# Kernel optimization log

Hardware: AMD Instinct MI355X
Metric: run time of the kernel (lower is better)

## Reference

```python
import jax, jax.numpy as jnp
import numpy as np

DIM = 1536
NHEADS = 12
HDIM = DIM // NHEADS  # 128
EPS = 1e-6
LOCAL_ATTN_SIZE = 3
SINK_SIZE = 1
MAX_ATTN = 32760 if LOCAL_ATTN_SIZE == -1 else LOCAL_ATTN_SIZE * 1560  # 4680


def _rms(x, g):
    # WanRMSNorm over last dim
    return x * jax.lax.rsqrt(jnp.mean(x * x, axis=-1, keepdims=True) + EPS) * g


def _rope(x, f, h, w, fr, fi, start_frame):
    # x: [b, s, n, d] with s == f*h*w; fr/fi: [1024, d//2] real/imag of complex rotations
    b, s, n, d = x.shape
    c = d // 2
    c0 = c - 2 * (c // 3)
    c1 = c // 3
    fc = jax.lax.complex(fr, fi)  # [1024, c]
    xr = x.reshape(b, s, n, c, 2)
    xc = jax.lax.complex(xr[..., 0], xr[..., 1])  # [b, s, n, c]
    ff = fc[start_frame:start_frame + f, :c0]      # [f, c0]
    fh = fc[:h, c0:c0 + c1]                        # [h, c1]
    fw = fc[:w, c0 + c1:c0 + 2 * c1]               # [w, c1]
    freqs_i = jnp.concatenate([
        jnp.broadcast_to(ff[:, None, None, :], (f, h, w, c0)),
        jnp.broadcast_to(fh[None, :, None, :], (f, h, w, c1)),
        jnp.broadcast_to(fw[None, None, :, :], (f, h, w, c1)),
    ], axis=-1).reshape(1, s, 1, c)
    y = xc * freqs_i
    return jnp.stack([y.real, y.imag], axis=-1).reshape(b, s, n, d)


def _attn(q, k, v):
    # plain SDPA (decode path of the module uses no mask on the gathered window)
    scale = 1.0 / np.sqrt(q.shape[-1]).astype(np.float32)
    logits = jnp.einsum('bqnd,bknd->bnqk', q, k) * scale
    p = jax.nn.softmax(logits, axis=-1)
    return jnp.einsum('bnqk,bknd->bqnd', p, v)


def _forward(x, cache_k, cache_v, freqs_real, freqs_imag,
             wq, bq, wk, bk, wv, bv, wo, bo, gq, gk,
             f_frames, height, width, current_start, global_end_index, local_end_index):
    b, s, _ = x.shape
    n, d = NHEADS, HDIM
    frame_seqlen = height * width
    start_frame = current_start // frame_seqlen

    q = _rms(x @ wq + bq, gq).reshape(b, s, n, d)
    k = _rms(x @ wk + bk, gk).reshape(b, s, n, d)
    v = (x @ wv + bv).reshape(b, s, n, d)

    rq = _rope(q, f_frames, height, width, freqs_real, freqs_imag, start_frame)
    rk = _rope(k, f_frames, height, width, freqs_real, freqs_imag, start_frame)

    current_end = current_start + s
    sink_tokens = SINK_SIZE * frame_seqlen
    kv_size = cache_k.shape[1]
    is_recompute = (current_end <= global_end_index) and (current_start > 0)

    kc, vc = cache_k, cache_v
    if LOCAL_ATTN_SIZE != -1 and current_end > global_end_index and s + local_end_index > kv_size:
        # evict oldest non-sink tokens, roll the rest toward the sink region
        num_evicted = s + local_end_index - kv_size
        num_rolled = local_end_index - num_evicted - sink_tokens
        src = slice(sink_tokens + num_evicted, sink_tokens + num_evicted + num_rolled)
        kc = kc.at[:, sink_tokens:sink_tokens + num_rolled].set(jax.lax.stop_gradient(cache_k[:, src]))
        vc = vc.at[:, sink_tokens:sink_tokens + num_rolled].set(jax.lax.stop_gradient(cache_v[:, src]))
        new_local_end = local_end_index + current_end - global_end_index - num_evicted
    else:
        new_local_end = local_end_index + current_end - global_end_index
    local_start = new_local_end - s
    write_start = max(local_start, sink_tokens) if is_recompute else local_start
    off = max(0, write_start - local_start)
    wl = max(0, new_local_end - write_start)
    if wl > 0:
        kc = kc.at[:, write_start:new_local_end].set(rk[:, off:off + wl])
        vc = vc.at[:, write_start:new_local_end].set(v[:, off:off + wl])

    if sink_tokens > 0:
        budget = MAX_ATTN - sink_tokens
        if budget > 0:
            lo = max(sink_tokens, new_local_end - budget)
            kcat = jnp.concatenate([kc[:, :sink_tokens], kc[:, lo:new_local_end]], axis=1)
            vcat = jnp.concatenate([vc[:, :sink_tokens], vc[:, lo:new_local_end]], axis=1)
        else:
            kcat, vcat = kc[:, :sink_tokens], vc[:, :sink_tokens]
        o = _attn(rq, kcat, vcat)
    else:
        ws = max(0, new_local_end - MAX_ATTN)
        o = _attn(rq, kc[:, ws:new_local_end], vc[:, ws:new_local_end])

    return o.reshape(b, s, DIM) @ wo + bo


def setup_inputs() -> dict:
    key = jax.random.key(0)
    ks = jax.random.split(key, 12)
    B, S, CACHE = 1, 1560, 4680
    sc = 0.02
    # RoPE tables as unit-magnitude complex rotations
    ang = jax.random.uniform(ks[0], (1024, HDIM // 2), jnp.float32, 0.0, 2.0 * np.pi)
    return {
        'x': jax.random.normal(ks[1], (B, S, DIM), jnp.float32),
        'cache_k': jax.random.normal(ks[2], (B, CACHE, NHEADS, HDIM), jnp.float32),
        'cache_v': jax.random.normal(ks[3], (B, CACHE, NHEADS, HDIM), jnp.float32),
        'freqs_real': jnp.cos(ang),
        'freqs_imag': jnp.sin(ang),
        'wq': jax.random.normal(ks[4], (DIM, DIM), jnp.float32) * sc,
        'bq': jnp.zeros((DIM,), jnp.float32),
        'wk': jax.random.normal(ks[5], (DIM, DIM), jnp.float32) * sc,
        'bk': jnp.zeros((DIM,), jnp.float32),
        'wv': jax.random.normal(ks[6], (DIM, DIM), jnp.float32) * sc,
        'bv': jnp.zeros((DIM,), jnp.float32),
        'wo': jax.random.normal(ks[7], (DIM, DIM), jnp.float32) * sc,
        'bo': jnp.zeros((DIM,), jnp.float32),
        'gq': jnp.ones((DIM,), jnp.float32),
        'gk': jnp.ones((DIM,), jnp.float32),
        'f_frames': 1,
        'height': 30,
        'width': 52,
        'current_start': 4680,
        'global_end_index': 4680,
        'local_end_index': 4680,
    }


def reference(x, cache_k, cache_v, freqs_real, freqs_imag,
              wq, bq, wk, bk, wv, bv, wo, bo, gq, gk,
              f_frames, height, width, current_start, global_end_index, local_end_index):
    return _forward(x, cache_k, cache_v, freqs_real, freqs_imag,
                    wq, bq, wk, bk, wv, bv, wo, bo, gq, gk,
                    f_frames, height, width, current_start, global_end_index, local_end_index)
```

## Files before the change

### kernel.cpp

```cpp
#include <hip/hip_runtime.h>
#include <cstdint>
#include <cstddef>

typedef unsigned int  u32;
typedef unsigned short u16;
typedef short s16x8 __attribute__((ext_vector_type(8)));
typedef float f32x4 __attribute__((ext_vector_type(4)));

#define DIM     1536
#define NH      12
#define HD      128
#define SEQ     1560
#define MPAD    1664
#define NKV     4680
#define NKPAD   4736
#define ROLL0   3120
#define NQK     4608
#define START_FRAME 3
#define NEGINF  -3.0e4f
#define NSPLIT  5
#define SPLITKC 960

#define EXP2F(x) exp2f(x)

__device__ __forceinline__ u16 f2bf(float f){
  u32 u = __builtin_bit_cast(u32, f);
  u32 r = (u + 0x7fffu + ((u >> 16) & 1u)) >> 16;
  return (u16)r;
}

__global__ void k_pre(const float* __restrict__ x, u16* __restrict__ xp,
                      u16* __restrict__ Kc, u16* __restrict__ VT,
                      u16* __restrict__ Qr, u16* __restrict__ Opad,
                      float* __restrict__ sumsq){
  int b = blockIdx.x;
  if (b < 244){
    int i = b * 256 + threadIdx.x;
    uint4 z = make_uint4(0u, 0u, 0u, 0u);
    if (i < 10752){
      int h = i / 896, r = i % 896;
      ((uint4*)(Kc + ((size_t)h * NKPAD + NKV) * 128))[r] = z;
    } else if (i < 21504){
      int j = i - 10752; int row = j / 7, c = j % 7;
      ((uint4*)(VT + (size_t)row * NKPAD + NKV))[c] = z;
    } else if (i < 41472){
      int j = i - 21504; int h = j / 1664, r = j % 1664;
      ((uint4*)(Qr + ((size_t)h * MPAD + SEQ) * 128))[r] = z;
    } else if (i < 61440){
      int r = i - 41472;
      ((uint4*)(Opad + (size_t)SEQ * DIM))[r] = z;
    } else if (i < 62272){
      ((uint4*)sumsq)[i - 61440] = z;
    }
  } else {
    int i = (b - 244) * 256 + threadIdx.x;
    const int n_src = SEQ * DIM / 8;
    u16 o[8] = {0,0,0,0,0,0,0,0};
    if (i < n_src){
      float4 a = ((const float4*)x)[2*i];
      float4 c = ((const float4*)x)[2*i + 1];
      o[0]=f2bf(a.x); o[1]=f2bf(a.y); o[2]=f2bf(a.z); o[3]=f2bf(a.w);
      o[4]=f2bf(c.x); o[5]=f2bf(c.y); o[6]=f2bf(c.z); o[7]=f2bf(c.w);
    }
    uint4 v = make_uint4((u32)o[0]|((u32)o[1]<<16), (u32)o[2]|((u32)o[3]<<16),
                         (u32)o[4]|((u32)o[5]<<16), (u32)o[6]|((u32)o[7]<<16));
    ((uint4*)xp)[i] = v;
  }
}

__global__ void k_transpose_w(const float* __restrict__ wq, const float* __restrict__ wk,
                              const float* __restrict__ wv, const float* __restrict__ wo,
                              u16* __restrict__ WTqkv, u16* __restrict__ WTo){
  __shared__ u32 tile[64][65];
  int z = blockIdx.z;
  const float* w = (z==0)?wq:(z==1)?wk:(z==2)?wv:wo;
  u16* dst = (z < 3) ? (WTqkv + (size_t)z * DIM * DIM) : WTo;
  int r0 = blockIdx.x * 64, c0 = blockIdx.y * 64;
  int t = threadIdx.x;
  int rr = t >> 4, cg = t & 15;
#pragma unroll
  for (int i = 0; i < 4; i++){
    int r = rr + i * 16;
    float4 v = *(const float4*)(w + (size_t)(r0 + r) * DIM + c0 + cg * 4);
    tile[r][cg*4+0] = f2bf(v.x); tile[r][cg*4+1] = f2bf(v.y);
    tile[r][cg*4+2] = f2bf(v.z); tile[r][cg*4+3] = f2bf(v.w);
  }
  __syncthreads();
  int c = t >> 2, rg = t & 3;
  u32 wds[8];
#pragma unroll
  for (int j = 0; j < 8; j++)
    wds[j] = (tile[rg*16 + 2*j][c] & 0xffffu) | (tile[rg*16 + 2*j + 1][c] << 16);
  u16* q = dst + (size_t)(c0 + c) * DIM + r0 + rg * 16;
  *(uint4*)q       = make_uint4(wds[0], wds[1], wds[2], wds[3]);
  *(uint4*)(q + 8) = make_uint4(wds[4], wds[5], wds[6], wds[7]);
}

#define LDK 40
__global__ __launch_bounds__(256) void k_gemm_qkv(
    const u16* __restrict__ A, const u16* __restrict__ B,
    const float* __restrict__ biasq, const float* __restrict__ biask, const float* __restrict__ biasv,
    float* __restrict__ Y, float* __restrict__ sumsq){
  __shared__ u16 As[128*LDK];
  __shared__ u16 Bs[128*LDK];
  int m0 = blockIdx.y * 128, n0 = blockIdx.x * 128;
  int t = threadIdx.x, w = t >> 6, lane = t & 63, quad = lane >> 4, lc = lane & 15;
  int wm = w & 1, wn = w >> 1;
  int sr = t >> 1, sh = (t & 1) * 16;
  f32x4 acc[4][4] = {};
  for (int kt = 0; kt < DIM/32; kt++){
    int k0 = kt * 32;
    __syncthreads();
    {
      const uint4* ga = (const uint4*)(A + (size_t)(m0 + sr) * DIM + k0 + sh);
      uint4 a0 = ga[0], a1 = ga[1];
      const uint4* gb = (const uint4*)(B + (size_t)(n0 + sr) * DIM + k0 + sh);
      uint4 b0 = gb[0], b1 = gb[1];
      *(uint4*)(As + sr * LDK + sh)     = a0;
      *(uint4*)(As + sr * LDK + sh + 8) = a1;
      *(uint4*)(Bs + sr * LDK + sh)     = b0;
      *(uint4*)(Bs + sr * LDK + sh + 8) = b1;
    }
    __syncthreads();
    s16x8 af[4], bf[4];
#pragma unroll
    for (int mt = 0; mt < 4; mt++) af[mt] = *(const s16x8*)(As + (wm*64 + mt*16 + lc) * LDK + quad * 8);
#pragma unroll
    for (int nt = 0; nt < 4; nt++) bf[nt] = *(const s16x8*)(Bs + (wn*64 + nt*16 + lc) * LDK + quad * 8);
#pragma unroll
    for (int mt = 0; mt < 4; mt++)
#pragma unroll
      for (int nt = 0; nt < 4; nt++)
        acc[mt][nt] = __builtin_amdgcn_mfma_f32_16x16x32_bf16(af[mt], bf[nt], acc[mt][nt], 0, 0, 0);
  }
  const float* bias; int cbase; int which;
  if (n0 < DIM)        { bias = biasq; cbase = 0;     which = 0; }
  else if (n0 < 2*DIM) { bias = biask; cbase = DIM;   which = 1; }
  else                 { bias = biasv; cbase = 2*DIM; which = 2; }
  float bvals[4];
#pragma unroll
  for (int nt = 0; nt < 4; nt++) bvals[nt] = bias[n0 - cbase + wn*64 + nt*16 + lc];
#pragma unroll
  for (int mt = 0; mt < 4; mt++){
    int row0 = m0 + wm*64 + mt*16 + quad*4;
    float ss[4] = {0.f, 0.f, 0.f, 0.f};
#pragma unroll
    for (int nt = 0; nt < 4; nt++){
      int col = n0 + wn*64 + nt*16 + lc;
#pragma unroll
      for (int r = 0; r < 4; r++){
        float y = acc[mt][nt][r] + bvals[nt];
        Y[(size_t)(row0 + r) * NQK + col] = y;
        ss[r] += y * y;
      }
    }
    if (which < 2){
      float* dst = sumsq + (which ? MPAD : 0);
#pragma unroll
      for (int r = 0; r < 4; r++){
        float v = ss[r];
        v += __shfl_xor(v, 1); v += __shfl_xor(v, 2); v += __shfl_xor(v, 4); v += __shfl_xor(v, 8);
        if (lc == 0) atomicAdd(&dst[row0 + r], v);
      }
    }
  }
}

__global__ void k_rope_qk(const float* __restrict__ Y, const float* __restrict__ sumsq,
                          const float* __restrict__ gq, const float* __restrict__ gk,
                          const float* __restrict__ fre, const float* __restrict__ fim,
                          u16* __restrict__ Qr, u16* __restrict__ Kc){
  int pos = blockIdx.x;
  int t = threadIdx.x;
  float scq = rsqrtf(sumsq[pos]        * (1.0f/1536.0f) + 1e-6f);
  float sck = rsqrtf(sumsq[MPAD + pos] * (1.0f/1536.0f) + 1e-6f);
  int hrow = pos / 52, wrow = pos % 52;
#pragma unroll
  for (int i = 0; i < 3; i++){
    int p = t + i * 256;
    int head = p >> 6, j = p & 63;
    int frow = (j < 22) ? START_FRAME : ((j < 43) ? hrow : wrow);
    float cr = fre[frow * 64 + j], ci = fim[frow * 64 + j];
    int d0 = head * 128 + 2 * j;
    float2 yq = *(const float2*)(Y + (size_t)pos * NQK + d0);
    float qa = yq.x * scq * gq[d0];
    float qb = yq.y * scq * gq[d0 + 1];
    u32 oq = (u32)f2bf(qa * cr - qb * ci) | ((u32)f2bf(qa * ci + qb * cr) << 16);
    *(u32*)(Qr + (size_t)(head * MPAD + pos) * 128 + 2 * j) = oq;
    float2 yk = *(const float2*)(Y + (size_t)pos * NQK + DIM + d0);
    float ka = yk.x * sck * gk[d0];
    float kb = yk.y * sck * gk[d0 + 1];
    u32 ok = (u32)f2bf(ka * cr - kb * ci) | ((u32)f2bf(ka * ci + kb * cr) << 16);
    *(u32*)(Kc + (size_t)(head * NKPAD + ROLL0 + pos) * 128 + 2 * j) = ok;
  }
}

__global__ void k_copy_cache_k(const float* __restrict__ ck, u16* __restrict__ Kc){
  int p = blockIdx.x;
  int src = (p < SEQ) ? p : p + SEQ;
  int t = threadIdx.x;
  int h = t >> 4, d = (t & 15) * 8;
  const float* s = ck + (size_t)src * DIM + t * 8;
  float4 a = ((const float4*)s)[0], b = ((const float4*)s)[1];
  uint4 v = make_uint4((u32)f2bf(a.x)|((u32)f2bf(a.y)<<16), (u32)f2bf(a.z)|((u32)f2bf(a.w)<<16),
                       (u32)f2bf(b.x)|((u32)f2bf(b.y)<<16), (u32)f2bf(b.z)|((u32)f2bf(b.w)<<16));
  *(uint4*)(Kc + (size_t)(h * NKPAD + p) * 128 + d) = v;
}

__global__ void k_tv_cache(const float* __restrict__ cv, u16* __restrict__ VT){
  __shared__ u32 tile[64][65];
  int p0 = blockIdx.x * 64, hd0 = blockIdx.y * 64;
  int t = threadIdx.x;
  int pr = t >> 4, cg = t & 15;
#pragma unroll
  for (int i = 0; i < 4; i++){
    int p = p0 + pr + i * 16;
    if (p < ROLL0){
      int src = (p < SEQ) ? p : p + SEQ;
      float4 v = *(const float4*)(cv + (size_t)src * DIM + hd0 + cg * 4);
      tile[pr + i*16][cg*4+0] = f2bf(v.x); tile[pr + i*16][cg*4+1] = f2bf(v.y);
      tile[pr + i*16][cg*4+2] = f2bf(v.z); tile[pr + i*16][cg*4+3] = f2bf(v.w);
    }
  }
  __syncthreads();
  int hd = t >> 2, pg = t & 3;
  int pbase = p0 + pg * 16;
  if (pbase < ROLL0){
    u32 wds[8];
#pragma unroll
    for (int j = 0; j < 8; j++)
      wds[j] = (tile[pg*16 + 2*j][hd] & 0xffffu) | (tile[pg*16 + 2*j + 1][hd] << 16);
    u16* q = VT + (size_t)(hd0 + hd) * NKPAD + pbase;
    *(uint4*)q       = make_uint4(wds[0], wds[1], wds[2], wds[3]);
    *(uint4*)(q + 8) = make_uint4(wds[4], wds[5], wds[6], wds[7]);
  }
}

__global__ void k_tv_new(const float* __restrict__ Y, u16* __restrict__ VT){
  __shared__ u32 tile[64][65];
  int p0 = blockIdx.x * 64, hd0 = blockIdx.y * 64;
  int t = threadIdx.x;
  int pr = t >> 4, cg = t & 15;
#pragma unroll
  for (int i = 0; i < 4; i++){
    int p = p0 + pr + i * 16;
    if (p < SEQ){
      float4 v = *(const float4*)(Y + (size_t)p * NQK + 2*DIM + hd0 + cg * 4);
      tile[pr + i*16][cg*4+0] = f2bf(v.x); tile[pr + i*16][cg*4+1] = f2bf(v.y);
      tile[pr + i*16][cg*4+2] = f2bf(v.z); tile[pr + i*16][cg*4+3] = f2bf(v.w);
    }
  }
  __syncthreads();
  int hd = t >> 2, pg = t & 3;
  int pbase = p0 + pg * 16;
  u32 wds[8];
#pragma unroll
  for (int j = 0; j < 8; j++)
    wds[j] = (tile[pg*16 + 2*j][hd] & 0xffffu) | (tile[pg*16 + 2*j + 1][hd] << 16);
  u16* q = VT + (size_t)(hd0 + hd) * NKPAD + ROLL0 + pbase;
  if (pbase + 8  <= SEQ) *(uint4*)q       = make_uint4(wds[0], wds[1], wds[2], wds[3]);
  if (pbase + 16 <= SEQ) *(uint4*)(q + 8) = make_uint4(wds[4], wds[5], wds[6], wds[7]);
}

#define LDKS 136
#define LDVS 68
#define LDPS 76
#define DEFER_THR 12.0f
__global__ __launch_bounds__(512, 4) void k_attn(const u16* __restrict__ Qr, const u16* __restrict__ Kc,
                                                 const u16* __restrict__ VT,
                                                 float* __restrict__ Opart, float* __restrict__ ml){
  __shared__ u16 Ks[64 * LDKS];
  __shared__ u16 Vs[128 * LDVS];
  __shared__ u16 Ps[8][16 * LDPS];
  int h = blockIdx.y, qb = blockIdx.x, sp = blockIdx.z;
  int t = threadIdx.x, w = t >> 6, lane = t & 63, quad = lane >> 4, lc = lane & 15;
  int qbase = qb * 128 + w * 16;
  const u16* Qbase = Qr + (size_t)(h * MPAD + qbase + lc) * 128;
  s16x8 qf[4];
#pragma unroll
  for (int kk = 0; kk < 4; kk++) qf[kk] = *(const s16x8*)(Qbase + kk * 32 + quad * 8);
  f32x4 oacc[8] = {};
  float m_[4] = {NEGINF, NEGINF, NEGINF, NEGINF};
  float l_[4] = {0.f, 0.f, 0.f, 0.f};
  const float scale = 0.08838834764831845f * 1.4426950408889634f;
  const u16* Kh = Kc + (size_t)h * NKPAD * 128;
  const u16* Vh = VT + (size_t)h * 128 * NKPAD;
  u16* Pw = &Ps[w][0];
  int kr0 = t >> 4,          kg0 = (t & 15) * 8;
  int kr1 = (t + 512) >> 4,  kg1 = ((t + 512) & 15) * 8;
  int vd0 = t >> 3,          vp0 = (t & 7) * 8;
  int vd1 = (t + 512) >> 3,  vp1 = ((t + 512) & 7) * 8;

  int kc0 = sp * SPLITKC;
  int kc1 = (sp == NSPLIT-1) ? NKPAD : kc0 + SPLITKC;
  uint4 kp0, kp1, vp0r, vp1r;
  {
    int kc = kc0;
    kp0  = *(const uint4*)(Kh + (size_t)(kc + kr0) * 128 + kg0);
    kp1  = *(const uint4*)(Kh + (size_t)(kc + kr1) * 128 + kg1);
    vp0r = *(const uint4*)(Vh + (size_t)vd0 * NKPAD + kc + vp0);
    vp1r = *(const uint4*)(Vh + (size_t)vd1 * NKPAD + kc + vp1);
  }
  for (int kc = kc0; kc < kc1; kc += 64){
    __syncthreads();
    *(uint4*)(Ks + kr0 * LDKS + kg0) = kp0;
    *(uint4*)(Ks + kr1 * LDKS + kg1) = kp1;
    *(uint4*)(Vs + vd0 * LDVS + vp0) = vp0r;
    *(uint4*)(Vs + vd1 * LDVS + vp1) = vp1r;
    __syncthreads();
    if (kc + 64 < kc1){
      int kn = kc + 64;
      kp0  = *(const uint4*)(Kh + (size_t)(kn + kr0) * 128 + kg0);
      kp1  = *(const uint4*)(Kh + (size_t)(kn + kr1) * 128 + kg1);
      vp0r = *(const uint4*)(Vh + (size_t)vd0 * NKPAD + kn + vp0);
      vp1r = *(const uint4*)(Vh + (size_t)vd1 * NKPAD + kn + vp1);
    }
    float s[4][4];
    __builtin_amdgcn_s_setprio(1);
#pragma unroll
    for (int nt = 0; nt < 4; nt++){
      f32x4 acc = {};
      int p = nt * 16 + lc;
#pragma unroll
      for (int kk = 0; kk < 4; kk++){
        s16x8 bfr = *(const s16x8*)(Ks + p * LDKS + (kk * 4 + quad) * 8);
        acc = __builtin_amdgcn_mfma_f32_16x16x32_bf16(qf[kk], bfr, acc, 0, 0, 0);
      }
#pragma unroll
      for (int r = 0; r < 4; r++) s[nt][r] = acc[r] * scale;
    }
    __builtin_amdgcn_s_setprio(0);
    if (kc + 64 > NKV){
#pragma unroll
      for (int nt = 0; nt < 4; nt++){
        int col = kc + nt * 16 + lc;
        if (col >= NKV){
#pragma unroll
          for (int r = 0; r < 4; r++) s[nt][r] = NEGINF;
        }
      }
    }
    float mx_[4];
    bool grow = false;
#pragma unroll
    for (int r = 0; r < 4; r++){
      float mx = fmaxf(fmaxf(s[0][r], s[1][r]), fmaxf(s[2][r], s[3][r]));
      mx = fmaxf(mx, __shfl_xor(mx, 1)); mx = fmaxf(mx, __shfl_xor(mx, 2));
      mx = fmaxf(mx, __shfl_xor(mx, 4)); mx = fmaxf(mx, __shfl_xor(mx, 8));
      mx_[r] = mx;
      grow = grow || (mx > m_[r] + DEFER_THR);
    }
    if (__any((int)grow)){
      float alpha[4];
#pragma unroll
      for (int r = 0; r < 4; r++){
        float mnew = fmaxf(m_[r], mx_[r]);
        alpha[r] = EXP2F(m_[r] - mnew);
        m_[r] = mnew;
        l_[r] *= alpha[r];
      }
#pragma unroll
      for (int dt = 0; dt < 8; dt++){
        f32x4 oo = oacc[dt];
#pragma unroll
        for (int r = 0; r < 4; r++) oo[r] *= alpha[r];
        oacc[dt] = oo;
      }
    }
#pragma unroll
    for (int nt = 0; nt < 4; nt++)
#pragma unroll
      for (int r = 0; r < 4; r++) s[nt][r] = EXP2F(s[nt][r] - m_[r]);
#pragma unroll
    for (int r = 0; r < 4; r++){
      float sum = s[0][r] + s[1][r] + s[2][r] + s[3][r];
      sum += __shfl_xor(sum, 1); sum += __shfl_xor(sum, 2);
      sum += __shfl_xor(sum, 4); sum += __shfl_xor(sum, 8);
      l_[r] += sum;
    }
#pragma unroll
    for (int nt = 0; nt < 4; nt++)
#pragma unroll
      for (int r = 0; r < 4; r++){
        int row = quad * 4 + r;
        Pw[row * LDPS + nt * 16 + lc] = f2bf(s[nt][r]);
      }
    asm volatile("s_waitcnt lgkmcnt(0)" ::: "memory");
    s16x8 a0 = *(const s16x8*)(Pw + lc * LDPS + quad * 8);
    s16x8 a1 = *(const s16x8*)(Pw + lc * LDPS + 32 + quad * 8);
    __builtin_amdgcn_s_setprio(1);
#pragma unroll
    for (int dt = 0; dt < 8; dt++){
      int d = dt * 16 + lc;
      s16x8 v0 = *(const s16x8*)(Vs + d * LDVS + quad * 8);
      s16x8 v1 = *(const s16x8*)(Vs + d * LDVS + 32 + quad * 8);
      oacc[dt] = __builtin_amdgcn_mfma_f32_16x16x32_bf16(a0, v0, oacc[dt], 0, 0, 0);
      oacc[dt] = __builtin_amdgcn_mfma_f32_16x16x32_bf16(a1, v1, oacc[dt], 0, 0, 0);
    }
    __builtin_amdgcn_s_setprio(0);
  }
  float* Ob = Opart + ((size_t)(sp * NH + h) * SEQ) * 128;
  float* mlb = ml + ((size_t)(sp * NH + h) * SEQ) * 2;
#pragma unroll
  for (int dt = 0; dt < 8; dt++)
#pragma unroll
    for (int r = 0; r < 4; r++){
      int row = qbase + quad * 4 + r;
      if (row < SEQ) Ob[(size_t)row * 128 + dt * 16 + lc] = oacc[dt][r];
    }
  if (lc == 0){
#pragma unroll
    for (int r = 0; r < 4; r++){
      int row = qbase + quad * 4 + r;
      if (row < SEQ){
        mlb[row * 2 + 0] = m_[r];
        mlb[row * 2 + 1] = l_[r];
      }
    }
  }
}

__global__ void k_attn_cmb(const float* __restrict__ Opart, const float* __restrict__ ml,
                           u16* __restrict__ Og){
  int row = blockIdx.x, h = blockIdx.y, d = threadIdx.x;
  float m[NSPLIT], l[NSPLIT];
  float M = NEGINF;
#pragma unroll
  for (int s = 0; s < NSPLIT; s++){
    m[s] = ml[((size_t)(s * NH + h) * SEQ + row) * 2 + 0];
    l[s] = ml[((size_t)(s * NH + h) * SEQ + row) * 2 + 1];
    M = fmaxf(M, m[s]);
  }
  float L = 0.f, o = 0.f;
#pragma unroll
  for (int s = 0; s < NSPLIT; s++){
    float wgt = EXP2F(m[s] - M);
    L += wgt * l[s];
    o += wgt * Opart[((size_t)(s * NH + h) * SEQ + row) * 128 + d];
  }
  Og[(size_t)row * DIM + h * 128 + d] = f2bf(o / L);
}

__global__ __launch_bounds__(256) void k_gemm_out(const u16* __restrict__ A, const u16* __restrict__ B,
                                                  const float* __restrict__ bo, float* __restrict__ out){
  __shared__ u16 As[128*LDK];
  __shared__ u16 Bs[128*LDK];
  int m0 = blockIdx.y * 128, n0 = blockIdx.x * 128;
  int t = threadIdx.x, w = t >> 6, lane = t & 63, quad = lane >> 4, lc = lane & 15;
  int wm = w & 1, wn = w >> 1;
  int sr = t >> 1, sh = (t & 1) * 16;
  f32x4 acc[4][4] = {};
  for (int kt = 0; kt < DIM/32; kt++){
    int k0 = kt * 32;
    __syncthreads();
    {
      const uint4* ga = (const uint4*)(A + (size_t)(m0 + sr) * DIM + k0 + sh);
      uint4 a0 = ga[0], a1 = ga[1];
      const uint4* gb = (const uint4*)(B + (size_t)(n0 + sr) * DIM + k0 + sh);
      uint4 b0 = gb[0], b1 = gb[1];
      *(uint4*)(As + sr * LDK + sh)     = a0;
      *(uint4*)(As + sr * LDK + sh + 8) = a1;
      *(uint4*)(Bs + sr * LDK + sh)     = b0;
      *(uint4*)(Bs + sr * LDK + sh + 8) = b1;
    }
    __syncthreads();
    s16x8 af[4], bf[4];
#pragma unroll
    for (int mt = 0; mt < 4; mt++) af[mt] = *(const s16x8*)(As + (wm*64 + mt*16 + lc) * LDK + quad * 8);
#pragma unroll
    for (int nt = 0; nt < 4; nt++) bf[nt] = *(const s16x8*)(Bs + (wn*64 + nt*16 + lc) * LDK + quad * 8);
#pragma unroll
    for (int mt = 0; mt < 4; mt++)
#pragma unroll
      for (int nt = 0; nt < 4; nt++)
        acc[mt][nt] = __builtin_amdgcn_mfma_f32_16x16x32_bf16(af[mt], bf[nt], acc[mt][nt], 0, 0, 0);
  }
  float bvals[4];
#pragma unroll
  for (int nt = 0; nt < 4; nt++) bvals[nt] = bo[n0 + wn*64 + nt*16 + lc];
#pragma unroll
  for (int mt = 0; mt < 4; mt++){
    int row0 = m0 + wm*64 + mt*16 + quad*4;
#pragma unroll
    for (int nt = 0; nt < 4; nt++){
      int col = n0 + wn*64 + nt*16 + lc;
#pragma unroll
      for (int r = 0; r < 4; r++){
        int row = row0 + r;
        if (row < SEQ) out[(size_t)row * DIM + col] = acc[mt][nt][r] + bvals[nt];
      }
    }
  }
}

extern "C" void kernel_launch(void* const* d_in, const int* in_sizes, int n_in,
                              void* d_out, int out_size, void* d_ws, size_t ws_size,
                              hipStream_t stream){
  const float* x   = (const float*)d_in[0];
  const float* ck  = (const float*)d_in[1];
  const float* cv  = (const float*)d_in[2];
  const float* fre = (const float*)d_in[3];
  const float* fim = (const float*)d_in[4];
  const float* wq  = (const float*)d_in[5];
  const float* bq  = (const float*)d_in[6];
  const float* wk  = (const float*)d_in[7];
  const float* bk  = (const float*)d_in[8];
  const float* wv  = (const float*)d_in[9];
  const float* bv  = (const float*)d_in[10];
  const float* wo  = (const float*)d_in[11];
  const float* bo  = (const float*)d_in[12];
  const float* gq  = (const float*)d_in[13];
  const float* gk  = (const float*)d_in[14];

  char* ws = (char*)d_ws;
  size_t off = 0;
  u16*   xpad  = (u16*)(ws + off);  off += (size_t)MPAD * DIM * 2;
  u16*   WTqkv = (u16*)(ws + off);  off += (size_t)3 * DIM * DIM * 2;
  float* Y     = (float*)(ws + off); off += (size_t)MPAD * NQK * 4;
  u16*   WTo   = (u16*)(ws + off);  off += (size_t)DIM * DIM * 2;
  float* sumsq = (float*)(ws + off); off += (size_t)2 * MPAD * 4;
  u16*   Qr    = (u16*)(ws + off);  off += (size_t)NH * MPAD * 128 * 2;
  u16*   Kc    = (u16*)(ws + off);  off += (size_t)NH * NKPAD * 128 * 2;
  u16*   VT    = (u16*)(ws + off);  off += (size_t)NH * 128 * NKPAD * 2;
  u16*   Opad  = (u16*)(ws + off);  off += (size_t)MPAD * DIM * 2;
  if (off > ws_size) return;
  float* Opart = (float*)ws;
  float* ml    = (float*)(ws + (size_t)NSPLIT * NH * SEQ * 128 * 4);

  k_pre         <<<dim3(1492), 256, 0, stream>>>(x, xpad, Kc, VT, Qr, Opad, sumsq);
  k_transpose_w <<<dim3(24, 24, 4), 256, 0, stream>>>(wq, wk, wv, wo, WTqkv, WTo);
  k_gemm_qkv    <<<dim3(NQK/128, MPAD/128), 256, 0, stream>>>(xpad, WTqkv, bq, bk, bv, Y, sumsq);
  k_rope_qk     <<<dim3(SEQ), 256, 0, stream>>>(Y, sumsq, gq, gk, fre, fim, Qr, Kc);
  k_copy_cache_k<<<dim3(ROLL0), 192, 0, stream>>>(ck, Kc);
  k_tv_cache    <<<dim3(49, 24), 256, 0, stream>>>(cv, VT);
  k_tv_new      <<<dim3(25, 24), 256, 0, stream>>>(Y, VT);
  k_attn        <<<dim3(MPAD/128, NH, NSPLIT), 512, 0, stream>>>(Qr, Kc, VT, Opart, ml);
  k_attn_cmb    <<<dim3(SEQ, NH), 128, 0, stream>>>(Opart, ml, Opad);
  k_gemm_out    <<<dim3(DIM/128, MPAD/128), 256, 0, stream>>>(Opad, WTo, bo, (float*)d_out);
}
```

Baseline: 439.7 us.

## Transpose QK^T MFMA and pass P via ds_bpermute instead of LDS

Swaps the MFMA operand order so each lane holds S^T with one query row per lane column. That turns the row max and sum reductions into two cross-quad shuffles with a single m/l per lane. The P tile is repacked into the PV A-operand with ds_bpermute register shuffles, which removes the per-wave LDS staging buffer and its waitcnt. The change also uses 4 KV splits instead of 5, different LDS padding strides, a lower defer threshold, and __expf in place of exp2f; the bpermute count and select logic add instructions and extra risk.

```diff
diff --git a/kernel.cpp b/kernel.cpp
--- a/kernel.cpp
+++ b/kernel.cpp
@@ -18,10 +18,8 @@
 #define NQK     4608
 #define START_FRAME 3
 #define NEGINF  -3.0e4f
-#define NSPLIT  5
-#define SPLITKC 960
-
-#define EXP2F(x) exp2f(x)
+#define NSPLIT  4
+#define SPLITKC 1216
 
 __device__ __forceinline__ u16 f2bf(float f){
   u32 u = __builtin_bit_cast(u32, f);
@@ -262,16 +260,14 @@
   if (pbase + 16 <= SEQ) *(uint4*)(q + 8) = make_uint4(wds[4], wds[5], wds[6], wds[7]);
 }
 
-#define LDKS 136
-#define LDVS 68
-#define LDPS 76
-#define DEFER_THR 12.0f
+#define LDKS 140
+#define LDVS 70
+#define DEFER_THR 8.0f
 __global__ __launch_bounds__(512, 4) void k_attn(const u16* __restrict__ Qr, const u16* __restrict__ Kc,
                                                  const u16* __restrict__ VT,
                                                  float* __restrict__ Opart, float* __restrict__ ml){
   __shared__ u16 Ks[64 * LDKS];
   __shared__ u16 Vs[128 * LDVS];
-  __shared__ u16 Ps[8][16 * LDPS];
   int h = blockIdx.y, qb = blockIdx.x, sp = blockIdx.z;
   int t = threadIdx.x, w = t >> 6, lane = t & 63, quad = lane >> 4, lc = lane & 15;
   int qbase = qb * 128 + w * 16;
@@ -280,40 +276,42 @@
 #pragma unroll
   for (int kk = 0; kk < 4; kk++) qf[kk] = *(const s16x8*)(Qbase + kk * 32 + quad * 8);
   f32x4 oacc[8] = {};
-  float m_[4] = {NEGINF, NEGINF, NEGINF, NEGINF};
-  float l_[4] = {0.f, 0.f, 0.f, 0.f};
-  const float scale = 0.08838834764831845f * 1.4426950408889634f;
+  float m_ = NEGINF;
+  float l_ = 0.f;
+  const float scale = 0.08838834764831845f;
   const u16* Kh = Kc + (size_t)h * NKPAD * 128;
   const u16* Vh = VT + (size_t)h * 128 * NKPAD;
-  u16* Pw = &Ps[w][0];
   int kr0 = t >> 4,          kg0 = (t & 15) * 8;
   int kr1 = (t + 512) >> 4,  kg1 = ((t + 512) & 15) * 8;
   int vd0 = t >> 3,          vp0 = (t & 7) * 8;
   int vd1 = (t + 512) >> 3,  vp1 = ((t + 512) & 7) * 8;
+  int aa = (lc + ((quad & 1) << 5)) << 2;
+  int ab = aa + 64;
+  int hi = quad >> 1;
 
   int kc0 = sp * SPLITKC;
   int kc1 = (sp == NSPLIT-1) ? NKPAD : kc0 + SPLITKC;
-  uint4 kp0, kp1, vp0r, vp1r;
+  uint4 kp0, kp1, vq0, vq1;
   {
     int kc = kc0;
-    kp0  = *(const uint4*)(Kh + (size_t)(kc + kr0) * 128 + kg0);
-    kp1  = *(const uint4*)(Kh + (size_t)(kc + kr1) * 128 + kg1);
-    vp0r = *(const uint4*)(Vh + (size_t)vd0 * NKPAD + kc + vp0);
-    vp1r = *(const uint4*)(Vh + (size_t)vd1 * NKPAD + kc + vp1);
+    kp0 = *(const uint4*)(Kh + (size_t)(kc + kr0) * 128 + kg0);
+    kp1 = *(const uint4*)(Kh + (size_t)(kc + kr1) * 128 + kg1);
+    vq0 = *(const uint4*)(Vh + (size_t)vd0 * NKPAD + kc + vp0);
+    vq1 = *(const uint4*)(Vh + (size_t)vd1 * NKPAD + kc + vp1);
   }
   for (int kc = kc0; kc < kc1; kc += 64){
     __syncthreads();
     *(uint4*)(Ks + kr0 * LDKS + kg0) = kp0;
     *(uint4*)(Ks + kr1 * LDKS + kg1) = kp1;
-    *(uint4*)(Vs + vd0 * LDVS + vp0) = vp0r;
-    *(uint4*)(Vs + vd1 * LDVS + vp1) = vp1r;
+    *(uint4*)(Vs + vd0 * LDVS + vp0) = vq0;
+    *(uint4*)(Vs + vd1 * LDVS + vp1) = vq1;
     __syncthreads();
     if (kc + 64 < kc1){
       int kn = kc + 64;
-      kp0  = *(const uint4*)(Kh + (size_t)(kn + kr0) * 128 + kg0);
-      kp1  = *(const uint4*)(Kh + (size_t)(kn + kr1) * 128 + kg1);
-      vp0r = *(const uint4*)(Vh + (size_t)vd0 * NKPAD + kn + vp0);
-      vp1r = *(const uint4*)(Vh + (size_t)vd1 * NKPAD + kn + vp1);
+      kp0 = *(const uint4*)(Kh + (size_t)(kn + kr0) * 128 + kg0);
+      kp1 = *(const uint4*)(Kh + (size_t)(kn + kr1) * 128 + kg1);
+      vq0 = *(const uint4*)(Vh + (size_t)vd0 * NKPAD + kn + vp0);
+      vq1 = *(const uint4*)(Vh + (size_t)vd1 * NKPAD + kn + vp1);
     }
     float s[4][4];
     __builtin_amdgcn_s_setprio(1);
@@ -323,8 +321,8 @@
       int p = nt * 16 + lc;
 #pragma unroll
       for (int kk = 0; kk < 4; kk++){
-        s16x8 bfr = *(const s16x8*)(Ks + p * LDKS + (kk * 4 + quad) * 8);
-        acc = __builtin_amdgcn_mfma_f32_16x16x32_bf16(qf[kk], bfr, acc, 0, 0, 0);
+        s16x8 kf = *(const s16x8*)(Ks + p * LDKS + (kk * 4 + quad) * 8);
+        acc = __builtin_amdgcn_mfma_f32_16x16x32_bf16(kf, qf[kk], acc, 0, 0, 0);
       }
 #pragma unroll
       for (int r = 0; r < 4; r++) s[nt][r] = acc[r] * scale;
@@ -333,61 +331,77 @@
     if (kc + 64 > NKV){
 #pragma unroll
       for (int nt = 0; nt < 4; nt++){
-        int col = kc + nt * 16 + lc;
-        if (col >= NKV){
-#pragma unroll
-          for (int r = 0; r < 4; r++) s[nt][r] = NEGINF;
-        }
-      }
-    }
-    float mx_[4];
-    bool grow = false;
-#pragma unroll
-    for (int r = 0; r < 4; r++){
-      float mx = fmaxf(fmaxf(s[0][r], s[1][r]), fmaxf(s[2][r], s[3][r]));
-      mx = fmaxf(mx, __shfl_xor(mx, 1)); mx = fmaxf(mx, __shfl_xor(mx, 2));
-      mx = fmaxf(mx, __shfl_xor(mx, 4)); mx = fmaxf(mx, __shfl_xor(mx, 8));
-      mx_[r] = mx;
-      grow = grow || (mx > m_[r] + DEFER_THR);
-    }
-    if (__any((int)grow)){
-      float alpha[4];
-#pragma unroll
-      for (int r = 0; r < 4; r++){
-        float mnew = fmaxf(m_[r], mx_[r]);
-        alpha[r] = EXP2F(m_[r] - mnew);
-        m_[r] = mnew;
-        l_[r] *= alpha[r];
-      }
+        int keyb = kc + nt * 16 + quad * 4;
+#pragma unroll
+        for (int r = 0; r < 4; r++) if (keyb + r >= NKV) s[nt][r] = NEGINF;
+      }
+    }
+    float mx = fmaxf(fmaxf(s[0][0], s[0][1]), fmaxf(s[0][2], s[0][3]));
+#pragma unroll
+    for (int nt = 1; nt < 4; nt++)
+      mx = fmaxf(mx, fmaxf(fmaxf(s[nt][0], s[nt][1]), fmaxf(s[nt][2], s[nt][3])));
+    mx = fmaxf(mx, __shfl_xor(mx, 16));
+    mx = fmaxf(mx, __shfl_xor(mx, 32));
+    if (__any(mx > m_ + DEFER_THR)){
+      float mnew = fmaxf(m_, mx);
+      float alpha = __expf(m_ - mnew);
+      m_ = mnew; l_ *= alpha;
+      float alr[4];
+#pragma unroll
+      for (int r = 0; r < 4; r++) alr[r] = __shfl(alpha, quad * 4 + r);
 #pragma unroll
       for (int dt = 0; dt < 8; dt++){
         f32x4 oo = oacc[dt];
 #pragma unroll
-        for (int r = 0; r < 4; r++) oo[r] *= alpha[r];
+        for (int r = 0; r < 4; r++) oo[r] *= alr[r];
         oacc[dt] = oo;
       }
     }
 #pragma unroll
     for (int nt = 0; nt < 4; nt++)
 #pragma unroll
-      for (int r = 0; r < 4; r++) s[nt][r] = EXP2F(s[nt][r] - m_[r]);
-#pragma unroll
-    for (int r = 0; r < 4; r++){
-      float sum = s[0][r] + s[1][r] + s[2][r] + s[3][r];
-      sum += __shfl_xor(sum, 1); sum += __shfl_xor(sum, 2);
-      sum += __shfl_xor(sum, 4); sum += __shfl_xor(sum, 8);
-      l_[r] += sum;
-    }
-#pragma unroll
-    for (int nt = 0; nt < 4; nt++)
-#pragma unroll
-      for (int r = 0; r < 4; r++){
-        int row = quad * 4 + r;
-        Pw[row * LDPS + nt * 16 + lc] = f2bf(s[nt][r]);
-      }
-    asm volatile("s_waitcnt lgkmcnt(0)" ::: "memory");
-    s16x8 a0 = *(const s16x8*)(Pw + lc * LDPS + quad * 8);
-    s16x8 a1 = *(const s16x8*)(Pw + lc * LDPS + 32 + quad * 8);
+      for (int r = 0; r < 4; r++) s[nt][r] = __expf(s[nt][r] - m_);
+    float sum = (s[0][0] + s[0][1]) + (s[0][2] + s[0][3]);
+#pragma unroll
+    for (int nt = 1; nt < 4; nt++)
+      sum += (s[nt][0] + s[nt][1]) + (s[nt][2] + s[nt][3]);
+    sum += __shfl_xor(sum, 16);
+    sum += __shfl_xor(sum, 32);
+    l_ += sum;
+    u32 w01[4], w23[4];
+#pragma unroll
+    for (int nt = 0; nt < 4; nt++){
+      w01[nt] = (u32)f2bf(s[nt][0]) | ((u32)f2bf(s[nt][1]) << 16);
+      w23[nt] = (u32)f2bf(s[nt][2]) | ((u32)f2bf(s[nt][3]) << 16);
+    }
+    u32 x0, x1;
+    uint4 A0, A1;
+    x0 = (u32)__builtin_amdgcn_ds_bpermute(aa, (int)w01[0]);
+    x1 = (u32)__builtin_amdgcn_ds_bpermute(aa, (int)w01[1]);
+    A0.x = hi ? x1 : x0;
+    x0 = (u32)__builtin_amdgcn_ds_bpermute(aa, (int)w23[0]);
+    x1 = (u32)__builtin_amdgcn_ds_bpermute(aa, (int)w23[1]);
+    A0.y = hi ? x1 : x0;
+    x0 = (u32)__builtin_amdgcn_ds_bpermute(ab, (int)w01[0]);
+    x1 = (u32)__builtin_amdgcn_ds_bpermute(ab, (int)w01[1]);
+    A0.z = hi ? x1 : x0;
+    x0 = (u32)__builtin_amdgcn_ds_bpermute(ab, (int)w23[0]);
+    x1 = (u32)__builtin_amdgcn_ds_bpermute(ab, (int)w23[1]);
+    A0.w = hi ? x1 : x0;
+    x0 = (u32)__builtin_amdgcn_ds_bpermute(aa, (int)w01[2]);
+    x1 = (u32)__builtin_amdgcn_ds_bpermute(aa, (int)w01[3]);
+    A1.x = hi ? x1 : x0;
+    x0 = (u32)__builtin_amdgcn_ds_bpermute(aa, (int)w23[2]);
+    x1 = (u32)__builtin_amdgcn_ds_bpermute(aa, (int)w23[3]);
+    A1.y = hi ? x1 : x0;
+    x0 = (u32)__builtin_amdgcn_ds_bpermute(ab, (int)w01[2]);
+    x1 = (u32)__builtin_amdgcn_ds_bpermute(ab, (int)w01[3]);
+    A1.z = hi ? x1 : x0;
+    x0 = (u32)__builtin_amdgcn_ds_bpermute(ab, (int)w23[2]);
+    x1 = (u32)__builtin_amdgcn_ds_bpermute(ab, (int)w23[3]);
+    A1.w = hi ? x1 : x0;
+    s16x8 a0 = __builtin_bit_cast(s16x8, A0);
+    s16x8 a1 = __builtin_bit_cast(s16x8, A1);
     __builtin_amdgcn_s_setprio(1);
 #pragma unroll
     for (int dt = 0; dt < 8; dt++){
@@ -399,6 +413,12 @@
     }
     __builtin_amdgcn_s_setprio(0);
   }
+  float mr[4], lr[4];
+#pragma unroll
+  for (int r = 0; r < 4; r++){
+    mr[r] = __shfl(m_, quad * 4 + r);
+    lr[r] = __shfl(l_, quad * 4 + r);
+  }
   float* Ob = Opart + ((size_t)(sp * NH + h) * SEQ) * 128;
   float* mlb = ml + ((size_t)(sp * NH + h) * SEQ) * 2;
 #pragma unroll
@@ -413,8 +433,8 @@
     for (int r = 0; r < 4; r++){
       int row = qbase + quad * 4 + r;
       if (row < SEQ){
-        mlb[row * 2 + 0] = m_[r];
-        mlb[row * 2 + 1] = l_[r];
+        mlb[row * 2 + 0] = mr[r];
+        mlb[row * 2 + 1] = lr[r];
       }
     }
   }
@@ -434,7 +454,7 @@
   float L = 0.f, o = 0.f;
 #pragma unroll
   for (int s = 0; s < NSPLIT; s++){
-    float wgt = EXP2F(m[s] - M);
+    float wgt = __expf(m[s] - M);
     L += wgt * l[s];
     o += wgt * Opart[((size_t)(s * NH + h) * SEQ + row) * 128 + d];
   }
```

New measurement: 403.7 us. -8.2%, faster.
